# Optimization experiments

Hardware: AMD Instinct MI355X
Metric: run time of the kernel (lower is better)

## Reference

```python
import jax, jax.numpy as jnp
import numpy as np

B, P, N, C = 4, 12, 1024, 64  # batch, past window, nodes, channels (in==hidden==out)


def setup_inputs() -> dict:
    key = jax.random.key(0)
    k1, k2, k3, k4, k5, k6 = jax.random.split(key, 6)
    x = jax.random.normal(k1, (B, P, N, C), dtype=jnp.float32)
    # float adjacency mask in {0,1}; force self-loops so no softmax row is empty
    A = jax.random.randint(k2, (B, P, N, N), 0, 2).astype(jnp.float32)
    A = A.at[..., jnp.arange(N), jnp.arange(N)].set(1.0)
    # learned params (nn.Linear stores weight as [out, in]; y = x @ W.T)
    W_emb = jax.random.normal(k3, (C, C), dtype=jnp.float32) / jnp.sqrt(jnp.float32(C))
    a1 = jax.random.normal(k4, (C,), dtype=jnp.float32)
    a2 = jax.random.normal(k5, (C,), dtype=jnp.float32)
    W_lin = jax.random.normal(k6, (C, C), dtype=jnp.float32) / jnp.sqrt(jnp.float32(C))
    return {"x": x, "A": A, "W_emb": W_emb, "a1": a1, "a2": a2, "W_lin": W_lin}


def reference(x, A, W_emb, a1, a2, W_lin):
    # x_emb = emb(x)  (bias-free linear)
    x_emb = jnp.einsum('bpnc,hc->bpnh', x, W_emb)            # [B,P,N,H]
    s1 = x_emb @ a1                                           # [B,P,N]
    s2 = x_emb @ a2                                           # [B,P,N]
    # additive GAT scores: a1_i + a2_j, broadcast instead of repeat
    z = jax.nn.leaky_relu(s1[..., :, None] + s2[..., None, :], 0.01)  # [B,P,N,N]
    z = jnp.where(A == 0.0, -jnp.inf, z)
    pi = jax.nn.softmax(z, axis=-1)                           # masked attention
    agg = jnp.einsum('bpij,bpjc->bpic', pi, x)                # weighted aggregation
    out = jax.nn.sigmoid(jnp.einsum('bpic,oc->bpio', agg, W_lin))
    return (out, A)
```

## Files before the change

### kernel.cpp

```cpp
#include <hip/hip_runtime.h>

typedef __attribute__((ext_vector_type(8))) __bf16 bf16x8;
typedef __attribute__((ext_vector_type(4))) float f32x4;

#define N_ 1024
#define C_ 64
#define BP_ 48

static __device__ __forceinline__ unsigned short f2bf(float f) {
    __bf16 b = (__bf16)f;
    return __builtin_bit_cast(unsigned short, b);
}
static __device__ __forceinline__ unsigned int pack2(float a, float b) {
    return (unsigned int)f2bf(a) | ((unsigned int)f2bf(b) << 16);
}

__global__ __launch_bounds__(256) void gat_pre(
    const float* __restrict__ x, const float* __restrict__ Wemb,
    const float* __restrict__ a1, const float* __restrict__ a2,
    float* __restrict__ s1g, float* __restrict__ s2g,
    unsigned short* __restrict__ xP, float* __restrict__ M2part)
{
    __shared__ float xs[64][65];
    __shared__ float vs[2][64];
    const int t = threadIdx.x, l = t & 63, w = t >> 6;
    const int j0 = blockIdx.x * 64;
    const int bp = blockIdx.y;

    if (w == 0) {
        float v1 = 0.f, v2 = 0.f;
        #pragma unroll 8
        for (int h = 0; h < 64; ++h) {
            float we = Wemb[h * 64 + l];
            v1 = fmaf(a1[h], we, v1);
            v2 = fmaf(a2[h], we, v2);
        }
        vs[0][l] = v1; vs[1][l] = v2;
    }
    const float* xb = x + ((size_t)bp * N_ + j0) * C_;
    #pragma unroll
    for (int it = 0; it < 16; ++it)
        xs[it * 4 + w][l] = xb[(it * 4 + w) * C_ + l];
    __syncthreads();

    const int jr = t >> 2, c0 = (t & 3) * 16;
    float p1 = 0.f, p2 = 0.f;
    #pragma unroll
    for (int k = 0; k < 16; ++k) {
        float xv = xs[jr][c0 + k];
        p1 = fmaf(xv, vs[0][c0 + k], p1);
        p2 = fmaf(xv, vs[1][c0 + k], p2);
    }
    p1 += __shfl_xor(p1, 1); p1 += __shfl_xor(p1, 2);
    p2 += __shfl_xor(p2, 1); p2 += __shfl_xor(p2, 2);
    if ((l & 3) == 0) {
        s1g[bp * N_ + j0 + jr] = p1;
        s2g[bp * N_ + j0 + jr] = p2;
    }
    float m = p2;
    m = fmaxf(m, __shfl_xor(m, 4));
    m = fmaxf(m, __shfl_xor(m, 8));
    m = fmaxf(m, __shfl_xor(m, 16));
    m = fmaxf(m, __shfl_xor(m, 32));
    if (l == 0) M2part[bp * 64 + blockIdx.x * 4 + w] = m;

    const int c = t >> 2, part = t & 3;
    unsigned short* dstb = xP + (size_t)bp * C_ * N_ + (size_t)c * N_ + j0 +
                           (part >> 1) * 32 + (part & 1) * 4;
    #pragma unroll
    for (int m_ = 0; m_ < 4; ++m_) {
        unsigned int lo = pack2(xs[part * 16 + 4 * m_ + 0][c],
                                xs[part * 16 + 4 * m_ + 1][c]);
        unsigned int hi = pack2(xs[part * 16 + 4 * m_ + 2][c],
                                xs[part * 16 + 4 * m_ + 3][c]);
        *(uint2*)&dstb[m_ * 8] = make_uint2(lo, hi);
    }
}

#define SB() __builtin_amdgcn_sched_barrier(0)

__global__ __launch_bounds__(256, 3) void gat_fused(
    const float* __restrict__ Ag, float* __restrict__ outA,
    const unsigned short* __restrict__ xP,
    const float* __restrict__ s1g, const float* __restrict__ s2g,
    const float* __restrict__ M2part,
    const float* __restrict__ Wlin, float* __restrict__ out)
{
    __shared__ unsigned short aggLDS[4][16][72];
    __shared__ float s2lds[1024];
    __shared__ float lsLDS[4][16];

    const int t = threadIdx.x, l = t & 63, w = t >> 6;
    const int i15 = l & 15, q = l >> 4;
    const int bp = blockIdx.y;
    const int ibase = blockIdx.x * 64 + w * 16;

    *(f32x4*)&s2lds[4 * t] = *(const f32x4*)&s2g[bp * N_ + 4 * t];

    float m2v = M2part[bp * 64 + l];
    #pragma unroll
    for (int off = 32; off >= 1; off >>= 1)
        m2v = fmaxf(m2v, __shfl_xor(m2v, off));
    const float M2 = m2v;
    const float s1_l = s1g[bp * N_ + ibase + i15];
    const float zr = s1_l + M2;
    const float mv = fmaxf(zr, 0.01f * zr);

    __syncthreads();

    const float* Arow = Ag + ((size_t)bp * N_ + ibase + i15) * N_ + q * 4;
    float* oArow = outA + ((size_t)bp * N_ + ibase + i15) * N_ + q * 4;
    const unsigned short* xProw = xP + (size_t)bp * C_ * N_ + (size_t)i15 * N_ + q * 8;

    f32x4 acc[4] = {};
    float ls = 0.f;

    f32x4 Aa[4], Ab[4];
    bf16x8 Xa[8], Xb[8];

#define LOADX(Xc, kk) do {                                                    \
    _Pragma("unroll")                                                         \
    for (int nt = 0; nt < 4; ++nt)                                            \
        _Pragma("unroll")                                                     \
        for (int s = 0; s < 2; ++s)                                           \
            Xc[s * 4 + nt] = *(const bf16x8*)&xProw[(size_t)nt * 16 * N_ +    \
                                                    (kk) * 64 + s * 32];      \
    } while (0)

#define LOADA(Ax, kk) do {                                                    \
    const float* _p = Arow + (kk) * 64;                                       \
    _Pragma("unroll")                                                         \
    for (int g = 0; g < 4; ++g)                                               \
        Ax[g] = *(const f32x4*)(_p + g * 16);                                 \
    } while (0)

#define CONSUME(Ac, Xc, kk) do {                                              \
    const int jrel = (kk) * 64;                                               \
    \
    f32x4 Ev[4];                                                              \
    _Pragma("unroll")                                                         \
    for (int g = 0; g < 4; ++g) {                                             \
        const f32x4 s2v = *(const f32x4*)&s2lds[jrel + g * 16 + q * 4];       \
        _Pragma("unroll")                                                     \
        for (int r = 0; r < 4; ++r) {                                         \
            float zz = s1_l + s2v[r];                                         \
            zz = fmaxf(zz, 0.01f * zz);                                       \
            Ev[g][r] = __expf(zz - mv);                                       \
        }                                                                     \
    }                                                                         \
    SB();                                                                     \
            \
    f32x4 P[4];                                                               \
    _Pragma("unroll")                                                         \
    for (int g = 0; g < 4; ++g) {                                             \
        *(f32x4*)(oArow + jrel + g * 16) = Ac[g];                             \
        _Pragma("unroll")                                                     \
        for (int r = 0; r < 4; ++r) {                                         \
            P[g][r] = Ac[g][r] * Ev[g][r];                                    \
            ls += P[g][r];                                                    \
        }                                                                     \
    }                                                                         \
    uint4 u0 = make_uint4(pack2(P[0][0], P[0][1]), pack2(P[0][2], P[0][3]),   \
                          pack2(P[1][0], P[1][1]), pack2(P[1][2], P[1][3]));  \
    uint4 u1 = make_uint4(pack2(P[2][0], P[2][1]), pack2(P[2][2], P[2][3]),   \
                          pack2(P[3][0], P[3][1]), pack2(P[3][2], P[3][3]));  \
    bf16x8 af0 = __builtin_bit_cast(bf16x8, u0);                              \
    bf16x8 af1 = __builtin_bit_cast(bf16x8, u1);                              \
    _Pragma("unroll")                                                         \
    for (int nt = 0; nt < 4; ++nt)                                            \
        acc[nt] = __builtin_amdgcn_mfma_f32_16x16x32_bf16(af0, Xc[nt],        \
                                                          acc[nt], 0, 0, 0);  \
    _Pragma("unroll")                                                         \
    for (int nt = 0; nt < 4; ++nt)                                            \
        acc[nt] = __builtin_amdgcn_mfma_f32_16x16x32_bf16(af1, Xc[4 + nt],    \
                                                          acc[nt], 0, 0, 0);  \
    } while (0)

    LOADX(Xa, 0); LOADA(Aa, 0);
    #pragma unroll 1
    for (int k = 0; k < 16; k += 2) {
        SB();
        LOADX(Xb, k + 1); LOADA(Ab, k + 1);
        SB();
        CONSUME(Aa, Xa, k);
        SB();
        if (k + 2 < 16) { LOADX(Xa, k + 2); LOADA(Aa, k + 2); }
        SB();
        CONSUME(Ab, Xb, k + 1);
    }
    SB();
#undef LOADX
#undef LOADA
#undef CONSUME

    ls += __shfl_xor(ls, 16);
    ls += __shfl_xor(ls, 32);
    if (q == 0) lsLDS[w][i15] = ls;
    const f32x4 lsq = *(const f32x4*)&lsLDS[w][4 * q];

    unsigned short* aggl = &aggLDS[w][0][0];
    #pragma unroll
    for (int nt = 0; nt < 4; ++nt)
        #pragma unroll
        for (int r = 0; r < 4; ++r)
            aggl[(q * 4 + r) * 72 + nt * 16 + i15] = f2bf(acc[nt][r] / lsq[r]);

    f32x4 d2[4] = {};
    #pragma unroll
    for (int s = 0; s < 2; ++s) {
        bf16x8 af = *(const bf16x8*)&aggl[i15 * 72 + s * 32 + q * 8];
        #pragma unroll
        for (int nt = 0; nt < 4; ++nt) {
            const float* wp = Wlin + (size_t)(nt * 16 + i15) * C_ + s * 32 + q * 8;
            f32x4 w0 = *(const f32x4*)wp;
            f32x4 w1 = *(const f32x4*)(wp + 4);
            bf16x8 bfr;
            #pragma unroll
            for (int jj = 0; jj < 4; ++jj) { bfr[jj] = (__bf16)w0[jj]; bfr[4 + jj] = (__bf16)w1[jj]; }
            d2[nt] = __builtin_amdgcn_mfma_f32_16x16x32_bf16(af, bfr, d2[nt], 0, 0, 0);
        }
    }
    float* orow = out + ((size_t)bp * N_ + ibase) * C_;
    #pragma unroll
    for (int nt = 0; nt < 4; ++nt)
        #pragma unroll
        for (int r = 0; r < 4; ++r)
            orow[(size_t)(q * 4 + r) * C_ + nt * 16 + i15] =
                1.f / (1.f + __expf(-d2[nt][r]));
}

extern "C" void kernel_launch(void* const* d_in, const int* in_sizes, int n_in,
                              void* d_out, int out_size, void* d_ws, size_t ws_size,
                              hipStream_t stream) {
    const float* x    = (const float*)d_in[0];
    const float* Ag   = (const float*)d_in[1];
    const float* Wemb = (const float*)d_in[2];
    const float* a1   = (const float*)d_in[3];
    const float* a2   = (const float*)d_in[4];
    const float* Wlin = (const float*)d_in[5];
    float* out  = (float*)d_out;
    float* outA = out + (size_t)BP_ * N_ * C_;

    float* s1g = (float*)d_ws;
    float* s2g = s1g + BP_ * N_;
    float* M2part = s2g + BP_ * N_;
    unsigned short* xP = (unsigned short*)(M2part + BP_ * 64);

    gat_pre<<<dim3(16, BP_), dim3(256), 0, stream>>>(x, Wemb, a1, a2,
                                                     s1g, s2g, xP, M2part);
    gat_fused<<<dim3(16, BP_), dim3(256), 0, stream>>>(Ag, outA, xP, s1g, s2g,
                                                       M2part, Wlin, out);
}
```

Baseline: 396.0 us.

## Load adjacency rows coalesced and redistribute mask bits through LDS nibbles

The A tile is now loaded so that each group of 16 lanes reads a contiguous 256-byte row segment, replacing the previous per-lane strided pattern spread across 16 rows. The A copy to outA uses the same coalesced layout. Each lane packs its mask values into 4-bit nibbles in LDS, and after an lgkmcnt wait it reads back the nibbles that match the MFMA operand layout to select exp values. This improves global coalescing of the dominant A read/write traffic, at the cost of extra LDS traffic, an explicit wait, and a larger shared footprint that may lower occupancy.

```diff
diff --git a/kernel.cpp b/kernel.cpp
--- a/kernel.cpp
+++ b/kernel.cpp
@@ -86,6 +86,7 @@
     const float* __restrict__ M2part,
     const float* __restrict__ Wlin, float* __restrict__ out)
 {
+    __shared__ unsigned char nibs[4][16][260];
     __shared__ unsigned short aggLDS[4][16][72];
     __shared__ float s2lds[1024];
     __shared__ float lsLDS[4][16];
@@ -108,12 +109,15 @@
 
     __syncthreads();
 
-    const float* Arow = Ag + ((size_t)bp * N_ + ibase + i15) * N_ + q * 4;
-    float* oArow = outA + ((size_t)bp * N_ + ibase + i15) * N_ + q * 4;
+    const int pr = l >> 4;
+    const int pc = l & 15;
+    const float* Abase = Ag + ((size_t)bp * N_ + ibase) * N_;
+    float* oAbase = outA + ((size_t)bp * N_ + ibase) * N_;
     const unsigned short* xProw = xP + (size_t)bp * C_ * N_ + (size_t)i15 * N_ + q * 8;
 
     f32x4 acc[4] = {};
     float ls = 0.f;
+    const int q4 = q * 4;
 
     f32x4 Aa[4], Ab[4];
     bf16x8 Xa[8], Xb[8];
@@ -128,19 +132,19 @@
     } while (0)
 
 #define LOADA(Ax, kk) do {                                                    \
-    const float* _p = Arow + (kk) * 64;                                       \
-    _Pragma("unroll")                                                         \
-    for (int g = 0; g < 4; ++g)                                               \
-        Ax[g] = *(const f32x4*)(_p + g * 16);                                 \
+    _Pragma("unroll")                                                         \
+    for (int inst = 0; inst < 4; ++inst)                                      \
+        Ax[inst] = *(const f32x4*)(Abase + (size_t)(inst * 4 + pr) * N_ +     \
+                                   (kk) * 64 + pc * 4);                       \
     } while (0)
 
 #define CONSUME(Ac, Xc, kk) do {                                              \
     const int jrel = (kk) * 64;                                               \
-    \
+                   \
     f32x4 Ev[4];                                                              \
     _Pragma("unroll")                                                         \
     for (int g = 0; g < 4; ++g) {                                             \
-        const f32x4 s2v = *(const f32x4*)&s2lds[jrel + g * 16 + q * 4];       \
+        const f32x4 s2v = *(const f32x4*)&s2lds[jrel + g * 16 + q4];          \
         _Pragma("unroll")                                                     \
         for (int r = 0; r < 4; ++r) {                                         \
             float zz = s1_l + s2v[r];                                         \
@@ -149,14 +153,27 @@
         }                                                                     \
     }                                                                         \
     SB();                                                                     \
-            \
+         \
+    _Pragma("unroll")                                                         \
+    for (int inst = 0; inst < 4; ++inst) {                                    \
+        unsigned int nib = 0;                                                 \
+        _Pragma("unroll")                                                     \
+        for (int r = 0; r < 4; ++r)                                           \
+            nib |= (Ac[inst][r] != 0.f ? 1u : 0u) << r;                       \
+        nibs[w][inst * 4 + pr][(kk) * 16 + pc] = (unsigned char)nib;          \
+        *(f32x4*)(oAbase + (size_t)(inst * 4 + pr) * N_ + jrel + pc * 4) =    \
+            Ac[inst];                                                         \
+    }                                                                         \
+    asm volatile("s_waitcnt lgkmcnt(0)" ::: "memory");                        \
+    SB();                                                                     \
+                         \
     f32x4 P[4];                                                               \
     _Pragma("unroll")                                                         \
     for (int g = 0; g < 4; ++g) {                                             \
-        *(f32x4*)(oArow + jrel + g * 16) = Ac[g];                             \
+        const unsigned int nib = nibs[w][i15][(kk) * 16 + g * 4 + q];         \
         _Pragma("unroll")                                                     \
         for (int r = 0; r < 4; ++r) {                                         \
-            P[g][r] = Ac[g][r] * Ev[g][r];                                    \
+            P[g][r] = ((nib >> r) & 1u) ? Ev[g][r] : 0.f;                     \
             ls += P[g][r];                                                    \
         }                                                                     \
     }                                                                         \
```

After: 397.7 us. No clear change (+0.4%).
